# Performance work log

Hardware: AMD Instinct MI355X
Metric: run time of the kernel (lower is better)

Reference implementation:

```python
import jax, jax.numpy as jnp
import numpy as np

B, T, C, H = 2, 2048, 1024, 16
HD = C // H  # 64
EPS = 1e-5


def _ln(x, g, b):
    mu = jnp.mean(x, axis=-1, keepdims=True)
    var = jnp.var(x, axis=-1, keepdims=True)
    return (x - mu) * jax.lax.rsqrt(var + EPS) * g + b


def setup_inputs() -> dict:
    key = jax.random.key(0)
    ks = jax.random.split(key, 8)
    s = lambda n: 1.0 / np.sqrt(n)
    return {
        "x": jax.random.normal(ks[0], (B, T, C), dtype=jnp.float32),
        "ln1_g": jnp.ones((C,), jnp.float32), "ln1_b": jnp.zeros((C,), jnp.float32),
        "ln2_g": jnp.ones((C,), jnp.float32), "ln2_b": jnp.zeros((C,), jnp.float32),
        "w_in": jax.random.normal(ks[1], (C, 3 * C), jnp.float32) * s(C),
        "b_in": jnp.zeros((3 * C,), jnp.float32),
        "w_out": jax.random.normal(ks[2], (C, C), jnp.float32) * s(C),
        "b_out": jnp.zeros((C,), jnp.float32),
        "w_fc": jax.random.normal(ks[3], (C, 4 * C), jnp.float32) * s(C),
        "b_fc": jnp.zeros((4 * C,), jnp.float32),
        "w_proj": jax.random.normal(ks[4], (4 * C, C), jnp.float32) * s(4 * C),
        "b_proj": jnp.zeros((C,), jnp.float32),
    }


def reference(x, ln1_g, ln1_b, ln2_g, ln2_b, w_in, b_in, w_out, b_out,
              w_fc, b_fc, w_proj, b_proj):
    # --- residual 1: x + attn(ln1(x)) ---
    h = _ln(x, ln1_g, ln1_b)
    qkv = h @ w_in + b_in                          # (B,T,3C)
    # reshape to (B,T,H,3*HD) then chunk per head (matches torch code exactly)
    qkv = qkv.reshape(B, T, H, 3 * HD).transpose(0, 2, 1, 3)  # (B,H,T,3*HD)
    q, k, v = jnp.split(qkv, 3, axis=-1)           # each (B,H,T,HD)
    att = jnp.einsum('bhqd,bhkd->bhqk', q, k) / np.sqrt(HD)
    causal = jnp.tril(jnp.ones((T, T), bool))
    att = jnp.where(causal, att, -jnp.inf)
    att = jax.nn.softmax(att, axis=-1)
    o = jnp.einsum('bhqk,bhkd->bhqd', att, v)      # (B,H,T,HD)
    o = o.transpose(0, 2, 1, 3).reshape(B, T, C)
    x1 = x + (o @ w_out + b_out)
    # --- ln2 applied to residual stream, then residual 2 on top of ln2 output ---
    y = _ln(x1, ln2_g, ln2_b)
    mlp = jax.nn.gelu(y @ w_fc + b_fc, approximate=False) @ w_proj + b_proj
    return y + mlp
```

## Files before the change

### kernel.cpp

```cpp
#include <hip/hip_runtime.h>
#include <hip/hip_bf16.h>
#include <math.h>

typedef __bf16 bf16;
typedef __bf16 bf16x8 __attribute__((ext_vector_type(8)));
typedef __bf16 bf16x4 __attribute__((ext_vector_type(4)));
typedef float floatx4 __attribute__((ext_vector_type(4)));
typedef int intx4 __attribute__((ext_vector_type(4)));

#define B_ 2
#define T_ 2048
#define C_ 1024
#define H_ 16
#define HD_ 64

__device__ __forceinline__ void gload_lds16(const bf16* g, bf16* l) {
    __builtin_amdgcn_global_load_lds(
        (const __attribute__((address_space(1))) unsigned int*)(g),
        (__attribute__((address_space(3))) unsigned int*)(l), 16, 0, 0);
}

__global__ __launch_bounds__(256) void transpose_all(
        const float* __restrict__ w_in, const float* __restrict__ w_out,
        const float* __restrict__ w_fc, const float* __restrict__ w_proj,
        bf16* __restrict__ o_in, bf16* __restrict__ o_out,
        bf16* __restrict__ o_fc, bf16* __restrict__ o_proj) {
    __shared__ float shf[32 * 33];
    int t = blockIdx.x;
    int tid = threadIdx.x;
    const float* src; bf16* dst; int K, N, idx;
    if (t < 3072)      { src = w_in;   dst = o_in;   K = 1024; N = 3072; idx = t; }
    else if (t < 7168) { src = w_fc;   dst = o_fc;   K = 1024; N = 4096; idx = t - 3072; }
    else if (t < 8192) { src = w_out;  dst = o_out;  K = 1024; N = 1024; idx = t - 7168; }
    else               { src = w_proj; dst = o_proj; K = 4096; N = 1024; idx = t - 8192; }
    int ntx = N >> 5;
    int nt = (idx % ntx) * 32, kt = (idx / ntx) * 32;
    int tx = tid & 31, ty = tid >> 5;
    #pragma unroll
    for (int i = 0; i < 32; i += 8)
        shf[(ty + i) * 33 + tx] = src[(size_t)(kt + ty + i) * N + nt + tx];
    __syncthreads();
    #pragma unroll
    for (int i = 0; i < 32; i += 8)
        dst[(size_t)(nt + ty + i) * K + kt + tx] = (bf16)shf[tx * 33 + ty + i];
}

__global__ __launch_bounds__(256) void ln_kernel(const float* __restrict__ x,
                                                 const float* __restrict__ g,
                                                 const float* __restrict__ b,
                                                 bf16* __restrict__ out_b,
                                                 float* __restrict__ out_f) {
    int row = blockIdx.x;
    int tid = threadIdx.x;
    const float* xr = x + (size_t)row * C_;
    float4 v = ((const float4*)xr)[tid];
    float s  = v.x + v.y + v.z + v.w;
    float ss = v.x * v.x + v.y * v.y + v.z * v.z + v.w * v.w;
    #pragma unroll
    for (int off = 32; off; off >>= 1) {
        s  += __shfl_down(s, off);
        ss += __shfl_down(ss, off);
    }
    __shared__ float red[8];
    int wid = tid >> 6;
    if ((tid & 63) == 0) { red[wid] = s; red[wid + 4] = ss; }
    __syncthreads();
    s  = red[0] + red[1] + red[2] + red[3];
    ss = red[4] + red[5] + red[6] + red[7];
    float mean = s * (1.0f / C_);
    float var  = ss * (1.0f / C_) - mean * mean;
    float rstd = rsqrtf(var + 1e-5f);
    float4 gv = ((const float4*)g)[tid];
    float4 bv = ((const float4*)b)[tid];
    float o0 = (v.x - mean) * rstd * gv.x + bv.x;
    float o1 = (v.y - mean) * rstd * gv.y + bv.y;
    float o2 = (v.z - mean) * rstd * gv.z + bv.z;
    float o3 = (v.w - mean) * rstd * gv.w + bv.w;
    bf16x4 ob = { (bf16)o0, (bf16)o1, (bf16)o2, (bf16)o3 };
    ((bf16x4*)out_b)[(size_t)row * 256 + tid] = ob;
    if (out_f) {
        float4 of; of.x = o0; of.y = o1; of.z = o2; of.w = o3;
        ((float4*)out_f)[(size_t)row * 256 + tid] = of;
    }
}

__device__ __forceinline__ float gelu_fast(float x) {
    float z2 = 1.5957691216f * (x + 0.044715f * x * x * x);
    float e = __expf(z2);
    float t = 1.0f - 2.0f * __builtin_amdgcn_rcpf(e + 1.0f);
    return 0.5f * x * (1.0f + t);
}

#define BAR() do { __builtin_amdgcn_sched_barrier(0); __builtin_amdgcn_s_barrier(); __builtin_amdgcn_sched_barrier(0); } while (0)
#define VMC6() asm volatile("s_waitcnt vmcnt(6)" ::: "memory")
#define VMC0() asm volatile("s_waitcnt vmcnt(0)" ::: "memory")

#define LOAD_A(AS, QM) \
  { _Pragma("unroll") for (int i_ = 0; i_ < 4; i_++) { \
      const int r_ = wm128 + ((QM) * 4 + i_) * 16 + lm; \
      _Pragma("unroll") for (int kc_ = 0; kc_ < 2; kc_++) \
        aR[i_][kc_] = *(const bf16x8*)((AS) + r_ * 64 + ((((kc_ << 2) | quad) ^ (lm & 7)) << 3)); } }

#define LOAD_B(BS, QN) \
  { _Pragma("unroll") for (int j_ = 0; j_ < 2; j_++) { \
      const int r_ = wn64 + ((QN) * 2 + j_) * 16 + lm; \
      _Pragma("unroll") for (int kc_ = 0; kc_ < 2; kc_++) \
        bR[QN][j_][kc_] = *(const bf16x8*)((BS) + r_ * 64 + ((((kc_ << 2) | quad) ^ (lm & 7)) << 3)); } }

#define MFMA_Q(QM, QN) \
  { __builtin_amdgcn_s_setprio(1); \
    _Pragma("unroll") for (int i_ = 0; i_ < 4; i_++) \
    _Pragma("unroll") for (int j_ = 0; j_ < 2; j_++) \
    _Pragma("unroll") for (int kc_ = 0; kc_ < 2; kc_++) \
      acc[(QM) * 4 + i_][(QN) * 2 + j_] = __builtin_amdgcn_mfma_f32_16x16x32_bf16( \
          aR[i_][kc_], bR[QN][j_][kc_], acc[(QM) * 4 + i_][(QN) * 2 + j_], 0, 0, 0); \
    __builtin_amdgcn_s_setprio(0); }

#define STG(gb, lb, r0v, k0v) \
    gload_lds16((gb) + (size_t)((r0v) + sr8) * K + (k0v) + scb, (lb) + ((r0v) + wid * 8) * 64)

template<int MODE>
__global__ __launch_bounds__(512, 2) void gemm256(const bf16* __restrict__ A,
                                                  const bf16* __restrict__ Bt,
                                                  const float* __restrict__ bias,
                                                  void* __restrict__ out,
                                                  int M, int N, int K) {
    (void)M;
    __shared__ __align__(16) bf16 smem[4 * 256 * 64];
    bf16* As0 = smem;
    bf16* Bs0 = smem + 1 * 256 * 64;
    bf16* As1 = smem + 2 * 256 * 64;
    bf16* Bs1 = smem + 3 * 256 * 64;

    int ntn = N >> 8;
    int lin = blockIdx.x;
    int id  = (lin & 7) * (gridDim.x >> 3) + (lin >> 3);
    int mt = id / ntn, nt = id - mt * ntn;
    int m0 = mt << 8, n0 = nt << 8;

    int tid = threadIdx.x;
    int wid = __builtin_amdgcn_readfirstlane(tid >> 6);
    int lane = tid & 63;
    int lm = lane & 15, quad = lane >> 4;
    int wm128 = (wid & 1) * 128;
    int wn64  = (wid >> 1) * 64;

    const bf16* Ablk = A  + (size_t)m0 * K;
    const bf16* Bblk = Bt + (size_t)n0 * K;

    int sr8 = wid * 8 + (lane >> 3);
    int scb = ((lane & 7) ^ (lane >> 3)) << 3;

    floatx4 acc[8][4];
    #pragma unroll
    for (int f = 0; f < 8; f++)
        #pragma unroll
        for (int g = 0; g < 4; g++) { floatx4 z = {0.f, 0.f, 0.f, 0.f}; acc[f][g] = z; }
    bf16x8 aR[4][2], bR[2][2][2];

    int nI = K >> 7;

    STG(Ablk, As0, 0, 0);   STG(Ablk, As0, 64, 0);
    STG(Ablk, As0, 128, 0); STG(Ablk, As0, 192, 0);
    STG(Bblk, Bs0, 0, 0);   STG(Bblk, Bs0, 64, 0);
    STG(Bblk, Bs0, 128, 0); STG(Bblk, Bs0, 192, 0);
    STG(Ablk, As1, 0, 64);  STG(Ablk, As1, 128, 64);
    STG(Bblk, Bs1, 0, 64);  STG(Bblk, Bs1, 64, 64);
    STG(Ablk, As1, 64, 64); STG(Ablk, As1, 192, 64);
    VMC6();
    BAR();

    for (int it = 0; it < nI; it++) {
        int kE = (2 * it + 2) << 6;
        int kO = (2 * it + 3) << 6;
        int kT = (2 * it + 1) << 6;
        bool nl = (it + 1 < nI);
        LOAD_A(As0, 0); LOAD_B(Bs0, 0);
        STG(Bblk, Bs1, 128, kT); STG(Bblk, Bs1, 192, kT);
        BAR(); MFMA_Q(0, 0); BAR();
        LOAD_B(Bs0, 1);
        if (nl) { STG(Ablk, As0, 0, kE); STG(Ablk, As0, 128, kE); }
        BAR(); MFMA_Q(0, 1); BAR();
        LOAD_A(As0, 1);
        if (nl) { STG(Bblk, Bs0, 0, kE); STG(Bblk, Bs0, 64, kE); }
        BAR(); MFMA_Q(1, 0); BAR();
        if (nl) { STG(Ablk, As0, 64, kE); STG(Ablk, As0, 192, kE); }
        BAR(); MFMA_Q(1, 1);
        if (nl) { VMC6(); } else { VMC0(); }
        BAR();
        LOAD_A(As1, 0); LOAD_B(Bs1, 0);
        if (nl) { STG(Bblk, Bs0, 128, kE); STG(Bblk, Bs0, 192, kE); }
        BAR(); MFMA_Q(0, 0); BAR();
        LOAD_B(Bs1, 1);
        if (nl) { STG(Ablk, As1, 0, kO); STG(Ablk, As1, 128, kO); }
        BAR(); MFMA_Q(0, 1); BAR();
        LOAD_A(As1, 1);
        if (nl) { STG(Bblk, Bs1, 0, kO); STG(Bblk, Bs1, 64, kO); }
        BAR(); MFMA_Q(1, 0); BAR();
        if (nl) { STG(Ablk, As1, 64, kO); STG(Ablk, As1, 192, kO); }
        BAR(); MFMA_Q(1, 1);
        if (nl) { VMC6(); }
        BAR();
    }

    if (MODE == 0) {
        bf16* ob = (bf16*)out;
        #pragma unroll
        for (int f = 0; f < 8; f++) {
            int row0 = m0 + wm128 + f * 16 + quad * 4;
            #pragma unroll
            for (int g = 0; g < 4; g++) {
                int n = n0 + wn64 + g * 16 + lm;
                float bsn = bias[n];
                #pragma unroll
                for (int r = 0; r < 4; r++)
                    ob[(size_t)(row0 + r) * N + n] = (bf16)(acc[f][g][r] + bsn);
            }
        }
    } else {
        bf16* ob = (bf16*)out;
        bf16* patch = smem + wid * (64 * 68);
        #pragma unroll
        for (int h = 0; h < 2; h++) {
            #pragma unroll
            for (int ff = 0; ff < 4; ff++)
                #pragma unroll
                for (int g = 0; g < 4; g++) {
                    int n = n0 + wn64 + g * 16 + lm;
                    float bsn = bias[n];
                    #pragma unroll
                    for (int r = 0; r < 4; r++)
                        patch[(ff * 16 + quad * 4 + r) * 68 + g * 16 + lm] =
                            (bf16)gelu_fast(acc[h * 4 + ff][g][r] + bsn);
                }
            #pragma unroll
            for (int ff = 0; ff < 4; ff++)
                #pragma unroll
                for (int kc = 0; kc < 2; kc++) {
                    bf16x8 v = *(const bf16x8*)&patch[(ff * 16 + lm) * 68 + kc * 32 + quad * 8];
                    size_t row = (size_t)(m0 + wm128 + h * 64 + ff * 16 + lm);
                    *(bf16x8*)(ob + row * N + n0 + wn64 + kc * 32 + quad * 8) = v;
                }
        }
    }
}

#define VMCP(n) asm volatile("s_waitcnt vmcnt(" #n ")" ::: "memory")

#define STGP(kt) { bf16* bs_ = smem + ((kt) & 3) * 16384; \
    gload_lds16(Ab + (size_t)sr8 * K + (kt) * 64 + scb,        bs_ + (wid * 8) * 64); \
    gload_lds16(Ab + (size_t)(64 + sr8) * K + (kt) * 64 + scb, bs_ + (64 + wid * 8) * 64); \
    gload_lds16(Bb + (size_t)sr8 * K + (kt) * 64 + scb,        bs_ + 8192 + (wid * 8) * 64); \
    gload_lds16(Bb + (size_t)(64 + sr8) * K + (kt) * 64 + scb, bs_ + 8192 + (64 + wid * 8) * 64); }

__global__ __launch_bounds__(512, 2) void gemm_npipe(const bf16* __restrict__ A,
                                                     const bf16* __restrict__ Bt,
                                                     const float* __restrict__ bias,
                                                     const float* __restrict__ add,
                                                     float* __restrict__ out,
                                                     int N, int K) {
    __shared__ __align__(16) bf16 smem[4 * 16384];
    int lin = blockIdx.x;
    int xcd = lin & 7, loc = lin >> 3;
    int m0 = (xcd * 4 + (loc & 3)) * 128;
    int n0 = (loc >> 2) * 128;
    int tid = threadIdx.x;
    int wid = __builtin_amdgcn_readfirstlane(tid >> 6);
    int lane = tid & 63;
    int lm = lane & 15, quad = lane >> 4;
    int wm32 = (wid & 3) * 32, wn64 = (wid >> 2) * 64;
    int sr8 = wid * 8 + (lane >> 3);
    int scb = ((lane & 7) ^ (lane >> 3)) << 3;
    const bf16* Ab = A  + (size_t)m0 * K;
    const bf16* Bb = Bt + (size_t)n0 * K;
    int NT = K >> 6;

    floatx4 acc[2][4];
    #pragma unroll
    for (int i = 0; i < 2; i++)
        #pragma unroll
        for (int j = 0; j < 4; j++) { floatx4 z = {0.f, 0.f, 0.f, 0.f}; acc[i][j] = z; }
    bf16x8 aR[2][2], bR[4][2];

    STGP(0); STGP(1); STGP(2);
    VMCP(8);
    BAR();

    for (int t = 0; t < NT; t++) {
        if (t + 3 < NT) STGP(t + 3);
        bf16* bs = smem + (t & 3) * 16384;
        #pragma unroll
        for (int i = 0; i < 2; i++)
            #pragma unroll
            for (int kc = 0; kc < 2; kc++)
                aR[i][kc] = *(const bf16x8*)(bs + (wm32 + i * 16 + lm) * 64 +
                                             ((((kc << 2) | quad) ^ (lm & 7)) << 3));
        #pragma unroll
        for (int j = 0; j < 4; j++)
            #pragma unroll
            for (int kc = 0; kc < 2; kc++)
                bR[j][kc] = *(const bf16x8*)(bs + 8192 + (wn64 + j * 16 + lm) * 64 +
                                             ((((kc << 2) | quad) ^ (lm & 7)) << 3));
        __builtin_amdgcn_s_setprio(1);
        #pragma unroll
        for (int kc = 0; kc < 2; kc++)
            #pragma unroll
            for (int i = 0; i < 2; i++)
                #pragma unroll
                for (int j = 0; j < 4; j++)
                    acc[i][j] = __builtin_amdgcn_mfma_f32_16x16x32_bf16(
                        aR[i][kc], bR[j][kc], acc[i][j], 0, 0, 0);
        __builtin_amdgcn_s_setprio(0);
        if (t + 3 < NT)      { VMCP(8); }
        else if (t == NT - 3){ VMCP(4); }
        else if (t == NT - 2){ VMCP(0); }
        BAR();
    }

    #pragma unroll
    for (int i = 0; i < 2; i++)
        #pragma unroll
        for (int j = 0; j < 4; j++) {
            int mbase = m0 + wm32 + i * 16 + quad * 4;
            int n     = n0 + wn64 + j * 16 + lm;
            float bsn = bias[n];
            #pragma unroll
            for (int r = 0; r < 4; r++) {
                size_t idx = (size_t)(mbase + r) * N + n;
                out[idx] = acc[i][j][r] + bsn + add[idx];
            }
        }
}

#define QT_ 128
#define KT_ 64

__device__ __forceinline__ void vt_stage(bf16* VtB, bf16x8 vv, int vdb,
                                         int vcolb, int oddf) {
    intx4 vi = *(intx4*)&vv;
    intx4 pi;
    #pragma unroll
    for (int m = 0; m < 4; m++) pi[m] = __shfl_xor(vi[m], 8);
    #pragma unroll
    for (int j = 0; j < 4; j++) {
        int w0 = j >> 1, sh = (j & 1) * 16;
        unsigned int oe = ((unsigned int)vi[w0] >> sh) & 0xffffu;
        unsigned int pe = ((unsigned int)pi[w0] >> sh) & 0xffffu;
        unsigned int oo = ((unsigned int)vi[2 + w0] >> sh) & 0xffffu;
        unsigned int po = ((unsigned int)pi[2 + w0] >> sh) & 0xffffu;
        unsigned int de = oe | (pe << 16);
        unsigned int dn = po | (oo << 16);
        unsigned int dw = oddf ? dn : de;
        *(unsigned int*)(VtB + (size_t)(vdb + j) * 72 + vcolb) = dw;
    }
}

__global__ __launch_bounds__(512) void attn_mfma_kernel(const bf16* __restrict__ qkv,
                                                        bf16* __restrict__ of) {
    int bh = blockIdx.x;
    int b = bh >> 4, h = bh & 15;
    int ny = gridDim.y;
    int gy = blockIdx.y;
    int yy = (gy < (ny >> 1)) ? gy : (ny + (ny >> 1) - 1 - gy);
    int q0 = (ny - 1 - yy) * QT_;
    int tid = threadIdx.x;
    int wid = __builtin_amdgcn_readfirstlane(tid >> 6);
    int lane = tid & 63;
    int lm = lane & 15, quad = lane >> 4;
    int sw = lm & 7;
    int r0 = q0 + wid * 16;

    const bf16* base = qkv + (size_t)b * T_ * (3 * C_) + h * (3 * HD_);

    __shared__ __align__(16) bf16 Ks[2][KT_][64];
    __shared__ __align__(16) bf16 Vt[2][HD_][72];
    __shared__ __align__(16) bf16 PsT[8][16][64];

    bf16x8 qf[2];
    #pragma unroll
    for (int kc = 0; kc < 2; kc++) {
        bf16x8 t = *(const bf16x8*)(base + (size_t)(r0 + lm) * (3 * C_) + kc * 32 + quad * 8);
        #pragma unroll
        for (int e = 0; e < 8; e++) t[e] = (bf16)((float)t[e] * 0.125f);
        qf[kc] = t;
    }

    floatx4 acc_o[4];
    #pragma unroll
    for (int dn = 0; dn < 4; dn++) { floatx4 z = {0.f, 0.f, 0.f, 0.f}; acc_o[dn] = z; }
    float mst = -1e30f, lst = 0.0f;

    int srow = tid >> 3;
    int scb  = ((lane & 7) ^ (lane >> 3)) << 3;
    int scol = (tid & 7) * 8;
    int oddf = srow & 1;
    int vcolb = (((srow >> 3) ^ (tid & 7)) << 3) + (srow & 6);
    int vdb   = scol + (oddf ? 4 : 0);

    int ntiles = q0 / KT_ + 2;

    {
        gload_lds16(base + (size_t)srow * (3 * C_) + HD_ + scb, &Ks[0][wid * 8][0]);
        bf16x8 vv = *(const bf16x8*)(base + (size_t)srow * (3 * C_) + 2 * HD_ + scol);
        vt_stage(&Vt[0][0][0], vv, vdb, vcolb, oddf);
        __syncthreads();
    }

    for (int t = 0; t < ntiles; t++) {
        int cur = t & 1;
        bool pre = (t + 1 < ntiles);
        bf16x8 vv;
        if (pre) {
            size_t nrow = (size_t)((t + 1) * KT_ + srow) * (3 * C_);
            gload_lds16(base + nrow + HD_ + scb, &Ks[cur ^ 1][wid * 8][0]);
            vv = *(const bf16x8*)(base + nrow + 2 * HD_ + scol);
        }
        __builtin_amdgcn_sched_barrier(0);

        int k0 = t * KT_;
        if (k0 <= r0 + 15) {
            floatx4 st[4];
            #pragma unroll
            for (int bn = 0; bn < 4; bn++) { floatx4 z = {0.f, 0.f, 0.f, 0.f}; st[bn] = z; }
            #pragma unroll
            for (int kc = 0; kc < 2; kc++) {
                bf16x8 kf[4];
                #pragma unroll
                for (int bn = 0; bn < 4; bn++)
                    kf[bn] = *(const bf16x8*)(&Ks[cur][bn * 16 + lm]
                                              [((((kc << 2) | quad) ^ sw) << 3)]);
                __builtin_amdgcn_s_setprio(1);
                #pragma unroll
                for (int bn = 0; bn < 4; bn++)
                    st[bn] = __builtin_amdgcn_mfma_f32_16x16x32_bf16(kf[bn], qf[kc], st[bn], 0, 0, 0);
                __builtin_amdgcn_s_setprio(0);
            }

            float vv_[4][4];
            float rm = -1e30f;
            if (k0 + KT_ - 1 > r0) {
                int gq = r0 + lm;
                #pragma unroll
                for (int bn = 0; bn < 4; bn++)
                    #pragma unroll
                    for (int r = 0; r < 4; r++) {
                        int key = k0 + bn * 16 + quad * 4 + r;
                        float sv = (key <= gq) ? st[bn][r] : -1e30f;
                        vv_[bn][r] = sv;
                        rm = fmaxf(rm, sv);
                    }
            } else {
                #pragma unroll
                for (int bn = 0; bn < 4; bn++)
                    #pragma unroll
                    for (int r = 0; r < 4; r++) {
                        vv_[bn][r] = st[bn][r];
                        rm = fmaxf(rm, st[bn][r]);
                    }
            }
            rm = fmaxf(rm, __shfl_xor(rm, 16));
            rm = fmaxf(rm, __shfl_xor(rm, 32));
            float mnew = fmaxf(mst, rm);
            float alpha = __expf(mst - mnew);
            mst = mnew;
            float ps = 0.f;
            #pragma unroll
            for (int bn = 0; bn < 4; bn++) {
                float p0 = __expf(vv_[bn][0] - mnew);
                float p1 = __expf(vv_[bn][1] - mnew);
                float p2 = __expf(vv_[bn][2] - mnew);
                float p3 = __expf(vv_[bn][3] - mnew);
                ps += (p0 + p1) + (p2 + p3);
                bf16x4 pk = { (bf16)p0, (bf16)p1, (bf16)p2, (bf16)p3 };
                int kb = bn * 2 + (quad >> 1);
                int col = ((kb ^ sw) << 3) + (quad & 1) * 4;
                *(bf16x4*)(&PsT[wid][lm][col]) = pk;
            }
            ps += __shfl_xor(ps, 16);
            ps += __shfl_xor(ps, 32);
            lst = lst * alpha + ps;

            #pragma unroll
            for (int r = 0; r < 4; r++) {
                float ar = __shfl(alpha, quad * 4 + r);
                #pragma unroll
                for (int dn = 0; dn < 4; dn++) acc_o[dn][r] *= ar;
            }

            __asm__ volatile("s_waitcnt lgkmcnt(0)" ::: "memory");

            #pragma unroll
            for (int kc = 0; kc < 2; kc++) {
                bf16x8 pa = *(const bf16x8*)(&PsT[wid][lm][((kc * 4 + quad) ^ sw) << 3]);
                bf16x8 vfr[4];
                #pragma unroll
                for (int dn = 0; dn < 4; dn++) {
                    int d = dn * 16 + lm;
                    int swd = (d >> 3) & 7;
                    vfr[dn] = *(const bf16x8*)(&Vt[cur][d][(((kc * 4 + quad) ^ swd) << 3)]);
                }
                __builtin_amdgcn_s_setprio(1);
                #pragma unroll
                for (int dn = 0; dn < 4; dn++)
                    acc_o[dn] = __builtin_amdgcn_mfma_f32_16x16x32_bf16(pa, vfr[dn], acc_o[dn], 0, 0, 0);
                __builtin_amdgcn_s_setprio(0);
            }
        }

        if (pre) vt_stage(&Vt[cur ^ 1][0][0], vv, vdb, vcolb, oddf);
        __syncthreads();
    }

    float il = 1.0f / lst;
    #pragma unroll
    for (int r = 0; r < 4; r++) {
        float ir = __shfl(il, quad * 4 + r);
        #pragma unroll
        for (int dn = 0; dn < 4; dn++)
            PsT[wid][quad * 4 + r][dn * 16 + lm] = (bf16)(acc_o[dn][r] * ir);
    }
    __asm__ volatile("s_waitcnt lgkmcnt(0)" ::: "memory");
    size_t rowg = (size_t)b * T_ + r0 + lm;
    #pragma unroll
    for (int kcl = 0; kcl < 2; kcl++) {
        bf16x8 v = *(const bf16x8*)&PsT[wid][lm][kcl * 32 + quad * 8];
        *(bf16x8*)(of + rowg * C_ + h * HD_ + kcl * 32 + quad * 8) = v;
    }
}

extern "C" void kernel_launch(void* const* d_in, const int* in_sizes, int n_in,
                              void* d_out, int out_size, void* d_ws, size_t ws_size,
                              hipStream_t stream) {
    (void)in_sizes; (void)n_in; (void)out_size; (void)ws_size;
    const float* x      = (const float*)d_in[0];
    const float* ln1_g  = (const float*)d_in[1];
    const float* ln1_b  = (const float*)d_in[2];
    const float* ln2_g  = (const float*)d_in[3];
    const float* ln2_b  = (const float*)d_in[4];
    const float* w_in   = (const float*)d_in[5];
    const float* b_in   = (const float*)d_in[6];
    const float* w_out  = (const float*)d_in[7];
    const float* b_out  = (const float*)d_in[8];
    const float* w_fc   = (const float*)d_in[9];
    const float* b_fc   = (const float*)d_in[10];
    const float* w_proj = (const float*)d_in[11];
    const float* b_proj = (const float*)d_in[12];

    char* ws = (char*)d_ws;
    const size_t MB = 1024 * 1024;
    bf16*  w_inT   = (bf16*)(ws + 0);
    bf16*  w_outT  = (bf16*)(ws + 6 * MB);
    bf16*  w_fcT   = (bf16*)(ws + 8 * MB);
    bf16*  w_projT = (bf16*)(ws + 16 * MB);
    bf16*  qkv     = (bf16*)(ws + 24 * MB);
    bf16*  fc_b    = (bf16*)(ws + 24 * MB);
    bf16*  o_b     = (bf16*)(ws + 56 * MB);
    bf16*  y_b     = (bf16*)(ws + 56 * MB);
    bf16*  h_b     = (bf16*)(ws + 64 * MB);
    float* x1      = (float*)(ws + 64 * MB);
    float* y_f     = (float*)(ws + 80 * MB);

    const int M = B_ * T_;

    transpose_all<<<12288, 256, 0, stream>>>(w_in, w_out, w_fc, w_proj,
                                             w_inT, w_outT, w_fcT, w_projT);

    ln_kernel<<<M, 256, 0, stream>>>(x, ln1_g, ln1_b, h_b, nullptr);
    gemm256<0><<<(M >> 8) * ((3 * C_) >> 8), 512, 0, stream>>>(h_b, w_inT, b_in,
                                                               qkv, M, 3 * C_, C_);
    attn_mfma_kernel<<<dim3(B_ * H_, T_ / QT_), 512, 0, stream>>>(qkv, o_b);
    gemm_npipe<<<256, 512, 0, stream>>>(o_b, w_outT, b_out, x, x1, C_, C_);
    ln_kernel<<<M, 256, 0, stream>>>(x1, ln2_g, ln2_b, y_b, y_f);
    gemm256<1><<<(M >> 8) * ((4 * C_) >> 8), 512, 0, stream>>>(y_b, w_fcT, b_fc,
                                                               fc_b, M, 4 * C_, C_);
    gemm_npipe<<<256, 512, 0, stream>>>(fc_b, w_projT, b_proj, y_f,
                                        (float*)d_out, C_, 4 * C_);
}
```

Before: 314.7 us.

## Shrink attention query tile to 64 rows with 4 waves, exp2 softmax

The attention kernel now uses 64-row query tiles with 256 threads (4 waves) instead of 128 rows and 8 waves. This doubles the grid and removes the wave-level skip of fully masked key tiles, since the tile count now matches the causal extent exactly. K/V staging is redistributed so each thread loads two rows or chunks, and the row-order interleave across blocks is rewritten for 32 tiles. The softmax scale log2(e)/8 is folded into Q so exp2f replaces __expf, which saves a multiply per exponent. The trade-off is finer load balance and more blocks against less K/V reuse per block, with the same load traffic now spread over fewer threads.

```diff
diff --git a/kernel.cpp b/kernel.cpp
--- a/kernel.cpp
+++ b/kernel.cpp
@@ -332,7 +332,7 @@
         }
 }
 
-#define QT_ 128
+#define QT_ 64
 #define KT_ 64
 
 __device__ __forceinline__ void vt_stage(bf16* VtB, bf16x8 vv, int vdb,
@@ -340,7 +340,7 @@
     intx4 vi = *(intx4*)&vv;
     intx4 pi;
     #pragma unroll
-    for (int m = 0; m < 4; m++) pi[m] = __shfl_xor(vi[m], 8);
+    for (int m = 0; m < 4; m++) pi[m] = __shfl_xor(vi[m], 4);
     #pragma unroll
     for (int j = 0; j < 4; j++) {
         int w0 = j >> 1, sh = (j & 1) * 16;
@@ -355,14 +355,14 @@
     }
 }
 
-__global__ __launch_bounds__(512) void attn_mfma_kernel(const bf16* __restrict__ qkv,
+__global__ __launch_bounds__(256) void attn_mfma_kernel(const bf16* __restrict__ qkv,
                                                         bf16* __restrict__ of) {
     int bh = blockIdx.x;
     int b = bh >> 4, h = bh & 15;
-    int ny = gridDim.y;
     int gy = blockIdx.y;
-    int yy = (gy < (ny >> 1)) ? gy : (ny + (ny >> 1) - 1 - gy);
-    int q0 = (ny - 1 - yy) * QT_;
+    int g = gy >> 3, hh = gy & 7;
+    int yy = (g == 0) ? hh : (g == 1) ? (15 - hh) : (g == 2) ? (16 + hh) : (31 - hh);
+    int q0 = (31 - yy) * QT_;
     int tid = threadIdx.x;
     int wid = __builtin_amdgcn_readfirstlane(tid >> 6);
     int lane = tid & 63;
@@ -374,14 +374,14 @@
 
     __shared__ __align__(16) bf16 Ks[2][KT_][64];
     __shared__ __align__(16) bf16 Vt[2][HD_][72];
-    __shared__ __align__(16) bf16 PsT[8][16][64];
+    __shared__ __align__(16) bf16 PsT[4][16][64];
 
     bf16x8 qf[2];
     #pragma unroll
     for (int kc = 0; kc < 2; kc++) {
         bf16x8 t = *(const bf16x8*)(base + (size_t)(r0 + lm) * (3 * C_) + kc * 32 + quad * 8);
         #pragma unroll
-        for (int e = 0; e < 8; e++) t[e] = (bf16)((float)t[e] * 0.125f);
+        for (int e = 0; e < 8; e++) t[e] = (bf16)((float)t[e] * 0.1803368801f);
         qf[kc] = t;
     }
 
@@ -390,35 +390,44 @@
     for (int dn = 0; dn < 4; dn++) { floatx4 z = {0.f, 0.f, 0.f, 0.f}; acc_o[dn] = z; }
     float mst = -1e30f, lst = 0.0f;
 
-    int srow = tid >> 3;
-    int scb  = ((lane & 7) ^ (lane >> 3)) << 3;
-    int scol = (tid & 7) * 8;
-    int oddf = srow & 1;
-    int vcolb = (((srow >> 3) ^ (tid & 7)) << 3) + (srow & 6);
-    int vdb   = scol + (oddf ? 4 : 0);
-
-    int ntiles = q0 / KT_ + 2;
+    int scb = ((lane & 7) ^ (lane >> 3)) << 3;
+    int vrow = wid * 16 + (lane >> 2);
+    int oddf = vrow & 1;
+
+    int ntiles = (q0 >> 6) + 1;
 
     {
-        gload_lds16(base + (size_t)srow * (3 * C_) + HD_ + scb, &Ks[0][wid * 8][0]);
-        bf16x8 vv = *(const bf16x8*)(base + (size_t)srow * (3 * C_) + 2 * HD_ + scol);
-        vt_stage(&Vt[0][0][0], vv, vdb, vcolb, oddf);
+        size_t kr = (size_t)(wid * 16 + (lane >> 3)) * (3 * C_);
+        gload_lds16(base + kr + HD_ + scb, &Ks[0][wid * 16][0]);
+        gload_lds16(base + kr + (size_t)8 * (3 * C_) + HD_ + scb, &Ks[0][wid * 16 + 8][0]);
+        size_t vr = (size_t)vrow * (3 * C_) + 2 * HD_;
+        #pragma unroll
+        for (int p = 0; p < 2; p++) {
+            int c_idx = (lane & 3) * 2 + p;
+            bf16x8 vv = *(const bf16x8*)(base + vr + c_idx * 8);
+            vt_stage(&Vt[0][0][0], vv, c_idx * 8 + (oddf ? 4 : 0),
+                     (((vrow >> 3) ^ c_idx) << 3) + (vrow & 6), oddf);
+        }
         __syncthreads();
     }
 
     for (int t = 0; t < ntiles; t++) {
         int cur = t & 1;
         bool pre = (t + 1 < ntiles);
-        bf16x8 vv;
+        bf16x8 vv0, vv1;
         if (pre) {
-            size_t nrow = (size_t)((t + 1) * KT_ + srow) * (3 * C_);
-            gload_lds16(base + nrow + HD_ + scb, &Ks[cur ^ 1][wid * 8][0]);
-            vv = *(const bf16x8*)(base + nrow + 2 * HD_ + scol);
+            size_t kr = (size_t)((t + 1) * KT_ + wid * 16 + (lane >> 3)) * (3 * C_);
+            gload_lds16(base + kr + HD_ + scb, &Ks[cur ^ 1][wid * 16][0]);
+            gload_lds16(base + kr + (size_t)8 * (3 * C_) + HD_ + scb,
+                        &Ks[cur ^ 1][wid * 16 + 8][0]);
+            size_t vr = (size_t)((t + 1) * KT_ + vrow) * (3 * C_) + 2 * HD_;
+            vv0 = *(const bf16x8*)(base + vr + ((lane & 3) * 2 + 0) * 8);
+            vv1 = *(const bf16x8*)(base + vr + ((lane & 3) * 2 + 1) * 8);
         }
         __builtin_amdgcn_sched_barrier(0);
 
         int k0 = t * KT_;
-        if (k0 <= r0 + 15) {
+        {
             floatx4 st[4];
             #pragma unroll
             for (int bn = 0; bn < 4; bn++) { floatx4 z = {0.f, 0.f, 0.f, 0.f}; st[bn] = z; }
@@ -441,35 +450,36 @@
             if (k0 + KT_ - 1 > r0) {
                 int gq = r0 + lm;
                 #pragma unroll
-                for (int bn = 0; bn < 4; bn++)
+                for (int bn = 0; bn < 4; bn++) {
                     #pragma unroll
                     for (int r = 0; r < 4; r++) {
                         int key = k0 + bn * 16 + quad * 4 + r;
-                        float sv = (key <= gq) ? st[bn][r] : -1e30f;
-                        vv_[bn][r] = sv;
-                        rm = fmaxf(rm, sv);
+                        vv_[bn][r] = (key <= gq) ? st[bn][r] : -1e30f;
                     }
+                    rm = fmaxf(rm, fmaxf(fmaxf(vv_[bn][0], vv_[bn][1]),
+                                         fmaxf(vv_[bn][2], vv_[bn][3])));
+                }
             } else {
                 #pragma unroll
-                for (int bn = 0; bn < 4; bn++)
+                for (int bn = 0; bn < 4; bn++) {
                     #pragma unroll
-                    for (int r = 0; r < 4; r++) {
-                        vv_[bn][r] = st[bn][r];
-                        rm = fmaxf(rm, st[bn][r]);
-                    }
+                    for (int r = 0; r < 4; r++) vv_[bn][r] = st[bn][r];
+                    rm = fmaxf(rm, fmaxf(fmaxf(vv_[bn][0], vv_[bn][1]),
+                                         fmaxf(vv_[bn][2], vv_[bn][3])));
+                }
             }
             rm = fmaxf(rm, __shfl_xor(rm, 16));
             rm = fmaxf(rm, __shfl_xor(rm, 32));
             float mnew = fmaxf(mst, rm);
-            float alpha = __expf(mst - mnew);
+            float alpha = exp2f(mst - mnew);
             mst = mnew;
             float ps = 0.f;
             #pragma unroll
             for (int bn = 0; bn < 4; bn++) {
-                float p0 = __expf(vv_[bn][0] - mnew);
-                float p1 = __expf(vv_[bn][1] - mnew);
-                float p2 = __expf(vv_[bn][2] - mnew);
-                float p3 = __expf(vv_[bn][3] - mnew);
+                float p0 = exp2f(vv_[bn][0] - mnew);
+                float p1 = exp2f(vv_[bn][1] - mnew);
+                float p2 = exp2f(vv_[bn][2] - mnew);
+                float p3 = exp2f(vv_[bn][3] - mnew);
                 ps += (p0 + p1) + (p2 + p3);
                 bf16x4 pk = { (bf16)p0, (bf16)p1, (bf16)p2, (bf16)p3 };
                 int kb = bn * 2 + (quad >> 1);
@@ -507,7 +517,12 @@
             }
         }
 
-        if (pre) vt_stage(&Vt[cur ^ 1][0][0], vv, vdb, vcolb, oddf);
+        if (pre) {
+            vt_stage(&Vt[cur ^ 1][0][0], vv0, ((lane & 3) * 2 + 0) * 8 + (oddf ? 4 : 0),
+                     (((vrow >> 3) ^ ((lane & 3) * 2 + 0)) << 3) + (vrow & 6), oddf);
+            vt_stage(&Vt[cur ^ 1][0][0], vv1, ((lane & 3) * 2 + 1) * 8 + (oddf ? 4 : 0),
+                     (((vrow >> 3) ^ ((lane & 3) * 2 + 1)) << 3) + (vrow & 6), oddf);
+        }
         __syncthreads();
     }
 
@@ -568,7 +583,7 @@
     ln_kernel<<<M, 256, 0, stream>>>(x, ln1_g, ln1_b, h_b, nullptr);
     gemm256<0><<<(M >> 8) * ((3 * C_) >> 8), 512, 0, stream>>>(h_b, w_inT, b_in,
                                                                qkv, M, 3 * C_, C_);
-    attn_mfma_kernel<<<dim3(B_ * H_, T_ / QT_), 512, 0, stream>>>(qkv, o_b);
+    attn_mfma_kernel<<<dim3(B_ * H_, T_ / QT_), 256, 0, stream>>>(qkv, o_b);
     gemm_npipe<<<256, 512, 0, stream>>>(o_b, w_outT, b_out, x, x1, C_, C_);
     ln_kernel<<<M, 256, 0, stream>>>(x1, ln2_g, ln2_b, y_b, y_f);
     gemm256<1><<<(M >> 8) * ((4 * C_) >> 8), 512, 0, stream>>>(y_b, w_fcT, b_fc,
```

Result: no change. 316.9 us (+0.7%).

## Split causal attention over key chunks with a separate combine kernel

Applied to the files above, without the earlier changes.

The attention kernel now splits each query tile's key range into chunks of up to 8 key tiles, giving 40 work items per head instead of 16. Each chunk writes an unnormalized partial output plus its running max and sum, and a new combine kernel merges them with log-sum-exp weights. The goal is to balance the causal triangle's uneven work and fill more CUs. It also folds log2(e) into the Q scale so exp2f replaces __expf. The cost is an extra launch, extra global traffic for the partials, and partial outputs rounded to bf16 before combining.

```diff
diff --git a/kernel.cpp b/kernel.cpp
--- a/kernel.cpp
+++ b/kernel.cpp
@@ -356,13 +356,20 @@
 }
 
 __global__ __launch_bounds__(512) void attn_mfma_kernel(const bf16* __restrict__ qkv,
-                                                        bf16* __restrict__ of) {
+                                                        bf16* __restrict__ Opart,
+                                                        float* __restrict__ mlw) {
     int bh = blockIdx.x;
     int b = bh >> 4, h = bh & 15;
-    int ny = gridDim.y;
-    int gy = blockIdx.y;
-    int yy = (gy < (ny >> 1)) ? gy : (ny + (ny >> 1) - 1 - gy);
-    int q0 = (ny - 1 - yy) * QT_;
+    int cy = blockIdx.y;
+    int y, ci;
+    if (cy < 4)       { y = cy;                   ci = 0; }
+    else if (cy < 12) { y = 4 + ((cy - 4) >> 1);  ci = (cy - 4) & 1; }
+    else if (cy < 24) { y = 8 + (cy - 12) / 3;    ci = (cy - 12) % 3; }
+    else              { y = 12 + ((cy - 24) >> 2); ci = (cy - 24) & 3; }
+    int q0 = y * QT_;
+    int tb = ci * 8;
+    int te = 2 * y + 2; if (te > tb + 8) te = tb + 8;
+
     int tid = threadIdx.x;
     int wid = __builtin_amdgcn_readfirstlane(tid >> 6);
     int lane = tid & 63;
@@ -381,7 +388,7 @@
     for (int kc = 0; kc < 2; kc++) {
         bf16x8 t = *(const bf16x8*)(base + (size_t)(r0 + lm) * (3 * C_) + kc * 32 + quad * 8);
         #pragma unroll
-        for (int e = 0; e < 8; e++) t[e] = (bf16)((float)t[e] * 0.125f);
+        for (int e = 0; e < 8; e++) t[e] = (bf16)((float)t[e] * 0.1803368801f);
         qf[kc] = t;
     }
 
@@ -397,18 +404,17 @@
     int vcolb = (((srow >> 3) ^ (tid & 7)) << 3) + (srow & 6);
     int vdb   = scol + (oddf ? 4 : 0);
 
-    int ntiles = q0 / KT_ + 2;
-
     {
-        gload_lds16(base + (size_t)srow * (3 * C_) + HD_ + scb, &Ks[0][wid * 8][0]);
-        bf16x8 vv = *(const bf16x8*)(base + (size_t)srow * (3 * C_) + 2 * HD_ + scol);
+        size_t gr = (size_t)(tb * KT_ + srow) * (3 * C_);
+        gload_lds16(base + gr + HD_ + scb, &Ks[0][wid * 8][0]);
+        bf16x8 vv = *(const bf16x8*)(base + gr + 2 * HD_ + scol);
         vt_stage(&Vt[0][0][0], vv, vdb, vcolb, oddf);
         __syncthreads();
     }
 
-    for (int t = 0; t < ntiles; t++) {
+    for (int t = tb; t < te; t++) {
         int cur = t & 1;
-        bool pre = (t + 1 < ntiles);
+        bool pre = (t + 1 < te);
         bf16x8 vv;
         if (pre) {
             size_t nrow = (size_t)((t + 1) * KT_ + srow) * (3 * C_);
@@ -441,35 +447,36 @@
             if (k0 + KT_ - 1 > r0) {
                 int gq = r0 + lm;
                 #pragma unroll
-                for (int bn = 0; bn < 4; bn++)
+                for (int bn = 0; bn < 4; bn++) {
                     #pragma unroll
                     for (int r = 0; r < 4; r++) {
                         int key = k0 + bn * 16 + quad * 4 + r;
-                        float sv = (key <= gq) ? st[bn][r] : -1e30f;
-                        vv_[bn][r] = sv;
-                        rm = fmaxf(rm, sv);
+                        vv_[bn][r] = (key <= gq) ? st[bn][r] : -1e30f;
                     }
+                    rm = fmaxf(rm, fmaxf(fmaxf(vv_[bn][0], vv_[bn][1]),
+                                         fmaxf(vv_[bn][2], vv_[bn][3])));
+                }
             } else {
                 #pragma unroll
-                for (int bn = 0; bn < 4; bn++)
+                for (int bn = 0; bn < 4; bn++) {
                     #pragma unroll
-                    for (int r = 0; r < 4; r++) {
-                        vv_[bn][r] = st[bn][r];
-                        rm = fmaxf(rm, st[bn][r]);
-                    }
+                    for (int r = 0; r < 4; r++) vv_[bn][r] = st[bn][r];
+                    rm = fmaxf(rm, fmaxf(fmaxf(vv_[bn][0], vv_[bn][1]),
+                                         fmaxf(vv_[bn][2], vv_[bn][3])));
+                }
             }
             rm = fmaxf(rm, __shfl_xor(rm, 16));
             rm = fmaxf(rm, __shfl_xor(rm, 32));
             float mnew = fmaxf(mst, rm);
-            float alpha = __expf(mst - mnew);
+            float alpha = exp2f(mst - mnew);
             mst = mnew;
             float ps = 0.f;
             #pragma unroll
             for (int bn = 0; bn < 4; bn++) {
-                float p0 = __expf(vv_[bn][0] - mnew);
-                float p1 = __expf(vv_[bn][1] - mnew);
-                float p2 = __expf(vv_[bn][2] - mnew);
-                float p3 = __expf(vv_[bn][3] - mnew);
+                float p0 = exp2f(vv_[bn][0] - mnew);
+                float p1 = exp2f(vv_[bn][1] - mnew);
+                float p2 = exp2f(vv_[bn][2] - mnew);
+                float p3 = exp2f(vv_[bn][3] - mnew);
                 ps += (p0 + p1) + (p2 + p3);
                 bf16x4 pk = { (bf16)p0, (bf16)p1, (bf16)p2, (bf16)p3 };
                 int kb = bn * 2 + (quad >> 1);
@@ -511,20 +518,88 @@
         __syncthreads();
     }
 
-    float il = 1.0f / lst;
     #pragma unroll
     for (int r = 0; r < 4; r++) {
-        float ir = __shfl(il, quad * 4 + r);
         #pragma unroll
         for (int dn = 0; dn < 4; dn++)
-            PsT[wid][quad * 4 + r][dn * 16 + lm] = (bf16)(acc_o[dn][r] * ir);
+            PsT[wid][quad * 4 + r][dn * 16 + lm] = (bf16)acc_o[dn][r];
     }
     __asm__ volatile("s_waitcnt lgkmcnt(0)" ::: "memory");
-    size_t rowg = (size_t)b * T_ + r0 + lm;
+    bf16* op = Opart + ((size_t)bh * 40 + cy) * (QT_ * HD_) + (wid * 16 + lm) * HD_;
     #pragma unroll
     for (int kcl = 0; kcl < 2; kcl++) {
         bf16x8 v = *(const bf16x8*)&PsT[wid][lm][kcl * 32 + quad * 8];
-        *(bf16x8*)(of + rowg * C_ + h * HD_ + kcl * 32 + quad * 8) = v;
+        *(bf16x8*)(op + kcl * 32 + quad * 8) = v;
+    }
+    if (lane < 16) {
+        float* mlp = mlw + (((size_t)bh * 40 + cy) * QT_ + wid * 16 + lane) * 2;
+        mlp[0] = mst;
+        mlp[1] = lst;
+    }
+}
+
+__global__ __launch_bounds__(256) void attn_combine(const bf16* __restrict__ Opart,
+                                                    const float* __restrict__ mlw,
+                                                    bf16* __restrict__ ob) {
+    int bh = blockIdx.x, y = blockIdx.y;
+    int b = bh >> 4, h = bh & 15;
+    int nc = (y >> 2) + 1;
+    int cy0 = (y < 4) ? y : (y < 8) ? (4 + ((y - 4) << 1))
+             : (y < 12) ? (12 + (y - 8) * 3) : (24 + ((y - 12) << 2));
+    int tid = threadIdx.x;
+    int row = tid >> 1, half = tid & 1;
+    size_t cbase = (size_t)bh * 40 + cy0;
+    const float* mlp = mlw + (cbase * QT_ + row) * 2;
+    float m0 = mlp[0], l0 = mlp[1];
+    float m1 = -1e30f, l1 = 0.f, m2 = -1e30f, l2 = 0.f, m3 = -1e30f, l3 = 0.f;
+    if (nc > 1) { m1 = mlp[2 * QT_];     l1 = mlp[2 * QT_ + 1]; }
+    if (nc > 2) { m2 = mlp[2 * 2 * QT_]; l2 = mlp[2 * 2 * QT_ + 1]; }
+    if (nc > 3) { m3 = mlp[3 * 2 * QT_]; l3 = mlp[3 * 2 * QT_ + 1]; }
+    float mx = fmaxf(fmaxf(m0, m1), fmaxf(m2, m3));
+    float s0 = exp2f(m0 - mx), s1 = exp2f(m1 - mx);
+    float s2 = exp2f(m2 - mx), s3 = exp2f(m3 - mx);
+    float wsum = s0 * l0 + s1 * l1 + s2 * l2 + s3 * l3;
+
+    const bf16* op = Opart + cbase * (QT_ * HD_) + row * HD_ + half * 32;
+    float acc[32];
+    #pragma unroll
+    for (int v8 = 0; v8 < 4; v8++) {
+        bf16x8 v = *(const bf16x8*)(op + v8 * 8);
+        #pragma unroll
+        for (int e = 0; e < 8; e++) acc[v8 * 8 + e] = s0 * (float)v[e];
+    }
+    if (nc > 1) {
+        #pragma unroll
+        for (int v8 = 0; v8 < 4; v8++) {
+            bf16x8 v = *(const bf16x8*)(op + QT_ * HD_ + v8 * 8);
+            #pragma unroll
+            for (int e = 0; e < 8; e++) acc[v8 * 8 + e] += s1 * (float)v[e];
+        }
+    }
+    if (nc > 2) {
+        #pragma unroll
+        for (int v8 = 0; v8 < 4; v8++) {
+            bf16x8 v = *(const bf16x8*)(op + 2 * QT_ * HD_ + v8 * 8);
+            #pragma unroll
+            for (int e = 0; e < 8; e++) acc[v8 * 8 + e] += s2 * (float)v[e];
+        }
+    }
+    if (nc > 3) {
+        #pragma unroll
+        for (int v8 = 0; v8 < 4; v8++) {
+            bf16x8 v = *(const bf16x8*)(op + 3 * QT_ * HD_ + v8 * 8);
+            #pragma unroll
+            for (int e = 0; e < 8; e++) acc[v8 * 8 + e] += s3 * (float)v[e];
+        }
+    }
+    float inv = 1.0f / wsum;
+    bf16* dst = ob + ((size_t)(b * T_ + y * QT_ + row)) * C_ + h * HD_ + half * 32;
+    #pragma unroll
+    for (int v8 = 0; v8 < 4; v8++) {
+        bf16x8 o;
+        #pragma unroll
+        for (int e = 0; e < 8; e++) o[e] = (bf16)(acc[v8 * 8 + e] * inv);
+        *(bf16x8*)(dst + v8 * 8) = o;
     }
 }
 
@@ -559,6 +634,8 @@
     bf16*  h_b     = (bf16*)(ws + 64 * MB);
     float* x1      = (float*)(ws + 64 * MB);
     float* y_f     = (float*)(ws + 80 * MB);
+    bf16*  Opart   = (bf16*)(ws + 64 * MB);
+    float* mlw     = (float*)(ws + 84 * MB);
 
     const int M = B_ * T_;
 
@@ -568,7 +645,8 @@
     ln_kernel<<<M, 256, 0, stream>>>(x, ln1_g, ln1_b, h_b, nullptr);
     gemm256<0><<<(M >> 8) * ((3 * C_) >> 8), 512, 0, stream>>>(h_b, w_inT, b_in,
                                                                qkv, M, 3 * C_, C_);
-    attn_mfma_kernel<<<dim3(B_ * H_, T_ / QT_), 512, 0, stream>>>(qkv, o_b);
+    attn_mfma_kernel<<<dim3(B_ * H_, 40), 512, 0, stream>>>(qkv, Opart, mlw);
+    attn_combine<<<dim3(B_ * H_, T_ / QT_), 256, 0, stream>>>(Opart, mlw, o_b);
     gemm_npipe<<<256, 512, 0, stream>>>(o_b, w_outT, b_out, x, x1, C_, C_);
     ln_kernel<<<M, 256, 0, stream>>>(x1, ln2_g, ln2_b, y_b, y_f);
     gemm256<1><<<(M >> 8) * ((4 * C_) >> 8), 512, 0, stream>>>(y_b, w_fcT, b_fc,
```

After: 329.5 us. 4.7% more time.
